# Optimization experiments

Hardware: AMD Instinct MI355X
Metric: run time of the kernel (lower is better)

## Reference

```python
import jax, jax.numpy as jnp
import numpy as np

N, E, R, H = 20000, 320000, 8, 4
KG, CC = 128, 4
IN, HID, OUT = 256, 256, 256  # in_channels = KG + 128 (GCN out)
HO1, HO2 = HID // H, OUT // H  # per-head out channels
SLOPE_ACT = 0.01   # nn.LeakyReLU default
SLOPE_ATT = 0.2    # RGATConv negative_slope default


def gcn_conv(x, W, b, src, dst):
    """PyG GCNConv: add self loops, symmetric norm, x@W, scatter-sum, +bias."""
    n = x.shape[0]
    loop = jnp.arange(n, dtype=src.dtype)
    s = jnp.concatenate([src, loop])
    d = jnp.concatenate([dst, loop])
    deg = jnp.zeros((n,), x.dtype).at[d].add(1.0)
    dis = jnp.where(deg > 0, jax.lax.rsqrt(jnp.maximum(deg, 1.0)), 0.0)
    norm = dis[s] * dis[d]                        # [E+N]
    h = x @ W                                     # [n, out]
    out = jax.ops.segment_sum(norm[:, None] * h[s], d, num_segments=n)
    return out + b


def rgat_conv(x, W, q, k, b, src, dst, edge_type, heads, oc):
    """PyG RGATConv (additive-self-attention, across-relation, dim=1, concat)."""
    n = x.shape[0]
    xw = jnp.einsum('ni,rio->rno', x, W)          # [R, n, heads*oc]
    out_i = xw[edge_type, dst]                    # [E, heads*oc]
    out_j = xw[edge_type, src]                    # [E, heads*oc]
    qi = out_i @ q                                # [E, heads]
    kj = out_j @ k                                # [E, heads]
    alpha = jax.nn.leaky_relu(qi + kj, SLOPE_ATT)
    # softmax over incoming edges per destination node (across-relation)
    amax = jax.ops.segment_max(alpha, dst, num_segments=n)[dst]
    ex = jnp.exp(alpha - amax)
    denom = jax.ops.segment_sum(ex, dst, num_segments=n)[dst]
    alpha = ex / denom                            # [E, heads]
    e = src.shape[0]
    msg = (alpha[:, :, None] * out_j.reshape(e, heads, oc)).reshape(e, heads * oc)
    out = jax.ops.segment_sum(msg, dst, num_segments=n) + b
    return out, alpha


def setup_inputs() -> dict:
    key = jax.random.key(0)
    ks = jax.random.split(key, 16)
    d = {}
    d['kg_emb'] = jax.random.normal(ks[0], (N, KG), jnp.float32)
    d['ccle0'] = jax.random.normal(ks[1], (N, CC), jnp.float32)
    d['gcn_w1'] = jax.random.normal(ks[2], (CC, 32), jnp.float32) / np.float32(np.sqrt(CC))
    d['gcn_b1'] = jnp.zeros((32,), jnp.float32)
    d['gcn_w2'] = jax.random.normal(ks[3], (32, 128), jnp.float32) / np.float32(np.sqrt(32))
    d['gcn_b2'] = jnp.zeros((128,), jnp.float32)
    d['rgat1_w'] = jax.random.normal(ks[4], (R, IN, HID), jnp.float32) / np.float32(np.sqrt(IN))
    d['rgat1_q'] = jax.random.normal(ks[5], (HID, H), jnp.float32) / np.float32(np.sqrt(HID))
    d['rgat1_k'] = jax.random.normal(ks[6], (HID, H), jnp.float32) / np.float32(np.sqrt(HID))
    d['rgat1_b'] = jnp.zeros((HID,), jnp.float32)
    d['rgat2_w'] = jax.random.normal(ks[7], (R, HID, OUT), jnp.float32) / np.float32(np.sqrt(HID))
    d['rgat2_q'] = jax.random.normal(ks[8], (OUT, H), jnp.float32) / np.float32(np.sqrt(OUT))
    d['rgat2_k'] = jax.random.normal(ks[9], (OUT, H), jnp.float32) / np.float32(np.sqrt(OUT))
    d['rgat2_b'] = jnp.zeros((OUT,), jnp.float32)
    d['lin_w'] = jax.random.normal(ks[10], (IN, OUT), jnp.float32) / np.float32(np.sqrt(IN))
    d['lin_b'] = jnp.zeros((OUT,), jnp.float32)
    d['edge_index'] = jax.random.randint(ks[11], (2, E), 0, N, jnp.int32)
    d['edge_type'] = jax.random.randint(ks[12], (E,), 0, R, jnp.int32)
    return d


def reference(kg_emb, ccle0, gcn_w1, gcn_b1, gcn_w2, gcn_b2,
              rgat1_w, rgat1_q, rgat1_k, rgat1_b,
              rgat2_w, rgat2_q, rgat2_k, rgat2_b,
              lin_w, lin_b, edge_index, edge_type):
    src, dst = edge_index[0], edge_index[1]
    # ccle_layer: GCN(4->32) -> LeakyReLU -> GCN(32->128)
    c = gcn_conv(ccle0, gcn_w1, gcn_b1, src, dst)
    c = jax.nn.leaky_relu(c, SLOPE_ACT)
    c = gcn_conv(c, gcn_w2, gcn_b2, src, dst)
    # node_id = arange(N): concat(kg_emb, ccle_out)
    x0 = jnp.concatenate([kg_emb, c], axis=1)     # [N, IN]
    h, a1 = rgat_conv(x0, rgat1_w, rgat1_q, rgat1_k, rgat1_b,
                      src, dst, edge_type, H, HO1)
    h = jax.nn.leaky_relu(h, SLOPE_ACT)           # dropout p=0 -> identity
    h, a2 = rgat_conv(h, rgat2_w, rgat2_q, rgat2_k, rgat2_b,
                      src, dst, edge_type, H, HO2)
    out = h + (x0 @ lin_w + lin_b)                # residual through self.lin
    return out, a1, a2
```

## Files before the change

### kernel.cpp

```cpp
#include <hip/hip_runtime.h>
#include <cstdint>

static constexpr int N = 20000;
static constexpr int E = 320000;
static constexpr int R = 8;
static constexpr int H = 4;
static constexpr int C = 256;

using short8 = __attribute__((ext_vector_type(8))) short;
using f32x4  = __attribute__((ext_vector_type(4))) float;

__device__ __forceinline__ float lrelu(float x, float s) { return x >= 0.f ? x : s * x; }
__device__ __forceinline__ unsigned short f2bf(float f) {
    unsigned u = __float_as_uint(f);
    unsigned r = (u + 0x7FFFu + ((u >> 16) & 1u)) >> 16;
    return (unsigned short)r;
}
__device__ __forceinline__ float bf2f(unsigned short s) {
    return __uint_as_float(((unsigned)s) << 16);
}

__global__ void k_zero_int(int* p, int n) {
    int i = blockIdx.x * blockDim.x + threadIdx.x;
    if (i < n) p[i] = 0;
}

__global__ void k_count(const int* __restrict__ ei, int* __restrict__ cnt) {
    int e = blockIdx.x * blockDim.x + threadIdx.x;
    if (e < E) atomicAdd(&cnt[ei[E + e]], 1);
}

__global__ __launch_bounds__(1024) void k_scan(const int* __restrict__ cnt,
                                               int* __restrict__ rowptr,
                                               int* __restrict__ cursor,
                                               float* __restrict__ dis) {
    __shared__ int part[1024];
    const int CH = (N + 1023) / 1024;
    int t = threadIdx.x;
    int base = t * CH;
    int sum = 0;
    for (int j = 0; j < CH; ++j) {
        int idx = base + j;
        if (idx < N) sum += cnt[idx];
    }
    part[t] = sum;
    __syncthreads();
    for (int off = 1; off < 1024; off <<= 1) {
        int v = 0;
        if (t >= off) v = part[t - off];
        __syncthreads();
        if (t >= off) part[t] += v;
        __syncthreads();
    }
    int run = part[t] - sum;
    for (int j = 0; j < CH; ++j) {
        int idx = base + j;
        if (idx < N) {
            int cv = cnt[idx];
            rowptr[idx] = run;
            cursor[idx] = run;
            dis[idx] = rsqrtf((float)cv + 1.0f);
            run += cv;
        }
    }
    if (t == 1023) rowptr[N] = part[1023];
}

__global__ void k_scatter(const int* __restrict__ ei, const int* __restrict__ et,
                          int* __restrict__ cursor, int* __restrict__ csr_se,
                          int* __restrict__ csr_eid) {
    int e = blockIdx.x * blockDim.x + threadIdx.x;
    if (e >= E) return;
    int d = ei[E + e];
    int pos = atomicAdd(&cursor[d], 1);
    csr_se[pos] = (et[e] << 16) | ei[e];
    csr_eid[pos] = e;
}

__global__ void k_h1(const float* __restrict__ x, const float* __restrict__ W,
                     float* __restrict__ h) {
    int idx = blockIdx.x * blockDim.x + threadIdx.x;
    if (idx >= N * 32) return;
    int n = idx >> 5, f = idx & 31;
    const float* xr = x + n * 4;
    float acc = 0.f;
#pragma unroll
    for (int c = 0; c < 4; ++c) acc += xr[c] * W[c * 32 + f];
    h[idx] = acc;
}

__global__ void k_agg32(const int* __restrict__ rowptr, const int* __restrict__ csr_se,
                        const float* __restrict__ dis, const float* __restrict__ h,
                        const float* __restrict__ b, float* __restrict__ c) {
    int idx = blockIdx.x * blockDim.x + threadIdx.x;
    if (idx >= N * 32) return;
    int d = idx >> 5, f = idx & 31;
    int beg = rowptr[d], end = rowptr[d + 1];
    float acc = 0.f;
    for (int i = beg; i < end; ++i) {
        int s = csr_se[i] & 0xFFFF;
        acc += dis[s] * h[s * 32 + f];
    }
    float dd = dis[d];
    c[idx] = dd * acc + dd * dd * h[idx] + b[f];
}

__global__ void k_h2kg(const float* __restrict__ c1, const float* __restrict__ W,
                       const float* __restrict__ kg, unsigned short* __restrict__ h,
                       float* __restrict__ x0, unsigned short* __restrict__ xb0) {
    int idx = blockIdx.x * blockDim.x + threadIdx.x;
    if (idx >= N * 128) return;
    int n = idx >> 7, f = idx & 127;
    const float* cr = c1 + n * 32;
    float acc = 0.f;
    for (int c = 0; c < 32; ++c) acc += lrelu(cr[c], 0.01f) * W[c * 128 + f];
    h[idx] = f2bf(acc);
    float v = kg[idx];
    x0[n * 256 + f] = v;
    xb0[n * 256 + f] = f2bf(v);
}

__global__ void k_agg128(const int* __restrict__ rowptr, const int* __restrict__ csr_se,
                         const float* __restrict__ dis,
                         const unsigned short* __restrict__ h,
                         const float* __restrict__ b, float* __restrict__ x0,
                         unsigned short* __restrict__ xb0) {
    int idx = blockIdx.x * blockDim.x + threadIdx.x;
    if (idx >= N * 128) return;
    int d = idx >> 7, f = idx & 127;
    int beg = rowptr[d], end = rowptr[d + 1];
    float acc = 0.f;
    int i = beg;
    for (; i + 2 <= end; i += 2) {
        int s0 = csr_se[i] & 0xFFFF;
        int s1 = csr_se[i + 1] & 0xFFFF;
        float d0 = dis[s0], d1 = dis[s1];
        float v0 = bf2f(h[s0 * 128 + f]), v1 = bf2f(h[s1 * 128 + f]);
        acc += d0 * v0 + d1 * v1;
    }
    if (i < end) {
        int s = csr_se[i] & 0xFFFF;
        acc += dis[s] * bf2f(h[s * 128 + f]);
    }
    float dd = dis[d];
    float v = dd * acc + dd * dd * bf2f(h[d * 128 + f]) + b[f];
    x0[d * 256 + 128 + f] = v;
    xb0[d * 256 + 128 + f] = f2bf(v);
}

__global__ __launch_bounds__(256) void k_wqkb(const float* __restrict__ W,
                                              const float* __restrict__ q,
                                              const float* __restrict__ kmat,
                                              unsigned short* __restrict__ wqkb) {
    int w = (blockIdx.x * blockDim.x + threadIdx.x) >> 6;
    int lane = threadIdx.x & 63;
    int r = w >> 8, i = w & 255;
    const float* wr = W + ((size_t)(r * 256 + i)) * 256;
    float4 a = *(const float4*)(wr + lane * 4);
    float aq0 = 0.f, aq1 = 0.f, aq2 = 0.f, aq3 = 0.f;
    float ak0 = 0.f, ak1 = 0.f, ak2 = 0.f, ak3 = 0.f;
    int o = lane * 4;
    const float av[4] = {a.x, a.y, a.z, a.w};
#pragma unroll
    for (int j = 0; j < 4; ++j) {
        float4 qv = *(const float4*)(q + (o + j) * 4);
        float4 kv = *(const float4*)(kmat + (o + j) * 4);
        aq0 += av[j] * qv.x; aq1 += av[j] * qv.y;
        aq2 += av[j] * qv.z; aq3 += av[j] * qv.w;
        ak0 += av[j] * kv.x; ak1 += av[j] * kv.y;
        ak2 += av[j] * kv.z; ak3 += av[j] * kv.w;
    }
#pragma unroll
    for (int d = 1; d < 64; d <<= 1) {
        aq0 += __shfl_xor(aq0, d); aq1 += __shfl_xor(aq1, d);
        aq2 += __shfl_xor(aq2, d); aq3 += __shfl_xor(aq3, d);
        ak0 += __shfl_xor(ak0, d); ak1 += __shfl_xor(ak1, d);
        ak2 += __shfl_xor(ak2, d); ak3 += __shfl_xor(ak3, d);
    }
    if (lane == 0) {
        int nq = r * 4, nk = 32 + r * 4;
        wqkb[(nq + 0) * 256 + i] = f2bf(aq0);
        wqkb[(nq + 1) * 256 + i] = f2bf(aq1);
        wqkb[(nq + 2) * 256 + i] = f2bf(aq2);
        wqkb[(nq + 3) * 256 + i] = f2bf(aq3);
        wqkb[(nk + 0) * 256 + i] = f2bf(ak0);
        wqkb[(nk + 1) * 256 + i] = f2bf(ak1);
        wqkb[(nk + 2) * 256 + i] = f2bf(ak2);
        wqkb[(nk + 3) * 256 + i] = f2bf(ak3);
    }
}

#define QP 264
__global__ __launch_bounds__(256) void k_qnkn_mfma(
    const unsigned short* __restrict__ xb, const unsigned short* __restrict__ wqkb,
    float* __restrict__ qn, float* __restrict__ kn)
{
    __shared__ unsigned short Ws[64 * QP];
    int t = threadIdx.x;
    {
        int r = t >> 2, off = (t & 3) * 64;
#pragma unroll
        for (int i = 0; i < 8; ++i)
            *(uint4*)(&Ws[r * QP + off + i * 8]) =
                *(const uint4*)(wqkb + r * 256 + off + i * 8);
    }
    __syncthreads();
    int wave = t >> 6, lane = t & 63;
    int lrow = lane & 15, kq = lane >> 4;
    int mw = blockIdx.x * 64 + wave * 16;
    int gm = mw + lrow;
    int gmc = gm < N ? gm : N - 1;

    f32x4 acc[4];
#pragma unroll
    for (int j = 0; j < 4; ++j) acc[j] = (f32x4){0.f, 0.f, 0.f, 0.f};

    for (int k0 = 0; k0 < 8; ++k0) {
        short8 af = *(const short8*)(xb + (size_t)gmc * 256 + k0 * 32 + kq * 8);
#pragma unroll
        for (int j = 0; j < 4; ++j) {
            short8 bf4 = *(const short8*)(&Ws[(j * 16 + lrow) * QP + k0 * 32 + kq * 8]);
            acc[j] = __builtin_amdgcn_mfma_f32_16x16x32_bf16(af, bf4, acc[j], 0, 0, 0);
        }
    }
#pragma unroll
    for (int j = 0; j < 4; ++j) {
        int col = j * 16 + lrow;
#pragma unroll
        for (int reg = 0; reg < 4; ++reg) {
            int gr = mw + kq * 4 + reg;
            if (gr < N) {
                if (col < 32) qn[gr * 32 + col] = acc[j][reg];
                else          kn[gr * 32 + (col - 32)] = acc[j][reg];
            }
        }
    }
}

__global__ void k_soft(const int* __restrict__ rowptr, const int* __restrict__ csr_se,
                       const int* __restrict__ csr_eid,
                       const float* __restrict__ qn, const float* __restrict__ kn,
                       float* __restrict__ alpha_csr, float* __restrict__ aout) {
    int wid = (blockIdx.x * blockDim.x + threadIdx.x) >> 6;
    int lane = threadIdx.x & 63;
    if (wid >= N) return;
    int d = wid;
    int beg = rowptr[d], end = rowptr[d + 1];
    if (beg >= end) return;
    int slot = lane >> 2, h = lane & 3;
    int nc = (end - beg + 15) >> 4;
    const float* qrow = qn + d * 32;

    auto rawv = [&](int i) {
        int se = csr_se[i];
        int tt = se >> 16, s = se & 0xFFFF;
        return lrelu(qrow[tt * 4 + h] + kn[s * 32 + tt * 4 + h], 0.2f);
    };

    float av[4];
    float m = -1e30f;
    for (int c = 0; c < nc; ++c) {
        int i = beg + c * 16 + slot;
        float v = (i < end) ? rawv(i) : -1e30f;
        if (c < 4) av[c] = v;
        m = fmaxf(m, v);
    }
    m = fmaxf(m, __shfl_xor(m, 4));
    m = fmaxf(m, __shfl_xor(m, 8));
    m = fmaxf(m, __shfl_xor(m, 16));
    m = fmaxf(m, __shfl_xor(m, 32));

    float sum = 0.f;
    for (int c = 0; c < nc; ++c) {
        int i = beg + c * 16 + slot;
        float ex = 0.f;
        if (i < end) {
            float v = (c < 4) ? av[c] : rawv(i);
            ex = expf(v - m);
        }
        if (c < 4) av[c] = ex;
        sum += ex;
    }
    sum += __shfl_xor(sum, 4);
    sum += __shfl_xor(sum, 8);
    sum += __shfl_xor(sum, 16);
    sum += __shfl_xor(sum, 32);
    float inv = 1.f / sum;

    for (int c = 0; c < nc; ++c) {
        int i = beg + c * 16 + slot;
        if (i < end) {
            float ex = (c < 4) ? av[c] : expf(rawv(i) - m);
            float a = ex * inv;
            alpha_csr[i * 4 + h] = a;
            aout[csr_eid[i] * 4 + h] = a;
        }
    }
}

#define WTP 72
__global__ __launch_bounds__(256) void k_wconv_t(const float* __restrict__ W,
                                                 unsigned short* __restrict__ Wt) {
    int bid = blockIdx.x;
    int z = bid >> 4;
    int tile = bid & 15;
    int k0 = (tile >> 2) * 64, n0 = (tile & 3) * 64;
    __shared__ unsigned short T[64 * WTP];
    int t = threadIdx.x;
    const float* Wz = W + ((size_t)z << 16);
    int r = t >> 4;
    int cs = (t & 15) * 4;
#pragma unroll
    for (int rr = 0; rr < 4; ++rr) {
        int k = r + rr * 16;
        float4 v = *(const float4*)(Wz + (size_t)(k0 + k) * 256 + n0 + cs);
        T[(cs + 0) * WTP + k] = f2bf(v.x);
        T[(cs + 1) * WTP + k] = f2bf(v.y);
        T[(cs + 2) * WTP + k] = f2bf(v.z);
        T[(cs + 3) * WTP + k] = f2bf(v.w);
    }
    __syncthreads();
    int n = t >> 2, ck = (t & 3) * 16;
    unsigned short* dst = Wt + ((size_t)z << 16) + (size_t)(n0 + n) * 256 + k0 + ck;
    const unsigned short* srcp = T + n * WTP + ck;
    *(uint4*)(dst) = *(const uint4*)(srcp);
    *(uint4*)(dst + 8) = *(const uint4*)(srcp + 8);
}

#define TM 128
#define TN 128
#define TK 32
#define LPP 40
__global__ __launch_bounds__(512) void gemm_mfma4(
    const unsigned short* __restrict__ A, const unsigned short* __restrict__ Bt,
    unsigned short* __restrict__ Cbf, float* __restrict__ Cf,
    const float* __restrict__ bias, const float* __restrict__ bias2,
    int M, int NZ, int NT, int MT, int zlin)
{
    __shared__ unsigned short As[TM * LPP];
    __shared__ unsigned short Bs[TN * LPP];

    int bi = blockIdx.x;
    int cx = bi & 7;
    int g = bi >> 3;
    int per = NZ * NT;
    int mh = g / per;
    int j  = g % per;
    int mt = mh * 8 + cx;
    if (mt >= MT) return;
    int z  = j % NZ;
    int nb = j / NZ;
    int m0 = mt * TM;
    int n0 = nb * TN;

    const unsigned short* Bz = Bt + ((size_t)z << 16);
    int t = threadIdx.x;
    int wave = t >> 6, lane = t & 63;
    int wr = wave >> 2;
    int wc = wave & 3;
    int lrow = lane & 15, kq = lane >> 4;
    int srow = t >> 2, skc = t & 3;

    f32x4 acc[4][2];
#pragma unroll
    for (int i = 0; i < 4; ++i)
#pragma unroll
        for (int jj = 0; jj < 2; ++jj) acc[i][jj] = (f32x4){0.f, 0.f, 0.f, 0.f};

    for (int k0 = 0; k0 < 256; k0 += TK) {
        {
            int gm = m0 + srow;
            uint4 va = {0, 0, 0, 0};
            if (gm < M) va = *(const uint4*)(A + (size_t)gm * 256 + k0 + skc * 8);
            *(uint4*)(&As[srow * LPP + skc * 8]) = va;
            uint4 vb = *(const uint4*)(Bz + (size_t)(n0 + srow) * 256 + k0 + skc * 8);
            *(uint4*)(&Bs[srow * LPP + skc * 8]) = vb;
        }
        __syncthreads();
        short8 af[4], bf4[2];
#pragma unroll
        for (int i = 0; i < 4; ++i)
            af[i] = *(const short8*)(&As[(wr * 64 + i * 16 + lrow) * LPP + kq * 8]);
#pragma unroll
        for (int jj = 0; jj < 2; ++jj)
            bf4[jj] = *(const short8*)(&Bs[(wc * 32 + jj * 16 + lrow) * LPP + kq * 8]);
#pragma unroll
        for (int i = 0; i < 4; ++i)
#pragma unroll
            for (int jj = 0; jj < 2; ++jj)
                acc[i][jj] = __builtin_amdgcn_mfma_f32_16x16x32_bf16(af[i], bf4[jj],
                                                                     acc[i][jj], 0, 0, 0);
        __syncthreads();
    }
    if (z == zlin) {
#pragma unroll
        for (int i = 0; i < 4; ++i)
#pragma unroll
            for (int jj = 0; jj < 2; ++jj) {
                int gn = n0 + wc * 32 + jj * 16 + lrow;
                float bsum = bias[gn] + bias2[gn];
#pragma unroll
                for (int reg = 0; reg < 4; ++reg) {
                    int gm = m0 + wr * 64 + i * 16 + kq * 4 + reg;
                    if (gm < M) Cf[(size_t)gm * 256 + gn] = acc[i][jj][reg] + bsum;
                }
            }
    } else {
#pragma unroll
        for (int i = 0; i < 4; ++i)
#pragma unroll
            for (int jj = 0; jj < 2; ++jj) {
                int gn = n0 + wc * 32 + jj * 16 + lrow;
#pragma unroll
                for (int reg = 0; reg < 4; ++reg) {
                    int gm = m0 + wr * 64 + i * 16 + kq * 4 + reg;
                    if (gm < M)
                        Cbf[((size_t)z * M + gm) * 256 + gn] = f2bf(acc[i][jj][reg]);
                }
            }
    }
}

__global__ __launch_bounds__(256) void k_msg_gather(
    const int* __restrict__ rowptr, const int* __restrict__ csr_se,
    const float* __restrict__ alpha_csr, const unsigned short* __restrict__ xw,
    const float* __restrict__ bias, float* __restrict__ out,
    unsigned short* __restrict__ xbout, int r0, int r1, int first, int act) {
    __shared__ float Pf[2][256];
    int tid = threadIdx.x;
    int wave = tid >> 6, lane = tid & 63;
    int nslot = wave >> 1, p = wave & 1;
    int node = blockIdx.x * 2 + nslot;
    int hsel = lane >> 4;
    float ax = 0.f, ay = 0.f, az = 0.f, aw = 0.f;

    auto edge = [&](int i) {
        int se = csr_se[i];
        int tt = se >> 16;
        if (tt >= r0 && tt < r1) {
            int s = se & 0xFFFF;
            float a = alpha_csr[i * 4 + hsel];
            uint2 pv = *(const uint2*)(xw + ((size_t)(tt - r0) * N + s) * 256 + lane * 4);
            ax += a * __uint_as_float(pv.x << 16);
            ay += a * __uint_as_float(pv.x & 0xFFFF0000u);
            az += a * __uint_as_float(pv.y << 16);
            aw += a * __uint_as_float(pv.y & 0xFFFF0000u);
        }
    };

    if (node < N) {
        int beg = rowptr[node], end = rowptr[node + 1];
        int i = beg + p;
        for (; i + 2 < end; i += 4) { edge(i); edge(i + 2); }
        if (i < end) edge(i);
    }
    if (p == 1) {
        float4 v = {ax, ay, az, aw};
        *(float4*)(&Pf[nslot][lane * 4]) = v;
    }
    __syncthreads();
    if (p == 0 && node < N) {
        float4 q = *(const float4*)(&Pf[nslot][lane * 4]);
        ax += q.x; ay += q.y; az += q.z; aw += q.w;
        float* o = out + (size_t)node * 256 + lane * 4;
        float vx, vy, vz, vw;
        if (first) {
            const float4 b = ((const float4*)bias)[lane];
            vx = ax + b.x; vy = ay + b.y; vz = az + b.z; vw = aw + b.w;
        } else {
            vx = o[0] + ax; vy = o[1] + ay; vz = o[2] + az; vw = o[3] + aw;
        }
        if (act) {
            vx = lrelu(vx, 0.01f); vy = lrelu(vy, 0.01f);
            vz = lrelu(vz, 0.01f); vw = lrelu(vw, 0.01f);
            unsigned short* xo = xbout + (size_t)node * 256 + lane * 4;
            xo[0] = f2bf(vx); xo[1] = f2bf(vy); xo[2] = f2bf(vz); xo[3] = f2bf(vw);
        }
        o[0] = vx; o[1] = vy; o[2] = vz; o[3] = vw;
    }
}

extern "C" void kernel_launch(void* const* d_in, const int* in_sizes, int n_in,
                              void* d_out, int out_size, void* d_ws, size_t ws_size,
                              hipStream_t stream) {
    const float* kg   = (const float*)d_in[0];
    const float* cc0  = (const float*)d_in[1];
    const float* gw1  = (const float*)d_in[2];
    const float* gb1  = (const float*)d_in[3];
    const float* gw2  = (const float*)d_in[4];
    const float* gb2  = (const float*)d_in[5];
    const float* r1w  = (const float*)d_in[6];
    const float* r1q  = (const float*)d_in[7];
    const float* r1k  = (const float*)d_in[8];
    const float* r1b  = (const float*)d_in[9];
    const float* r2w  = (const float*)d_in[10];
    const float* r2q  = (const float*)d_in[11];
    const float* r2k  = (const float*)d_in[12];
    const float* r2b  = (const float*)d_in[13];
    const float* linw = (const float*)d_in[14];
    const float* linb = (const float*)d_in[15];
    const int*   ei   = (const int*)d_in[16];
    const int*   et   = (const int*)d_in[17];

    float* out = (float*)d_out;
    float* a1  = out + (size_t)N * C;
    float* a2  = a1 + (size_t)E * H;

    float* ws = (float*)d_ws;
    size_t off = 0;
    float* dis  = ws + off; off += N;
    float* h1   = ws + off; off += (size_t)N * 32;
    float* c1   = ws + off; off += (size_t)N * 32;
    unsigned short* h2b = (unsigned short*)(ws + off); off += (size_t)N * 64;
    float* x0   = ws + off; off += (size_t)N * C;
    float* hmid = ws + off; off += (size_t)N * C;
    float* qn   = ws + off; off += (size_t)N * R * H;
    float* kn   = ws + off; off += (size_t)N * R * H;
    int* cnt     = (int*)(ws + off); off += N;
    int* rowptr  = (int*)(ws + off); off += N + 1;
    int* cursor  = (int*)(ws + off); off += N;
    int* csr_se  = (int*)(ws + off); off += E;
    int* csr_eid = (int*)(ws + off); off += E;
    float* alpha = ws + off; off += (size_t)E * H;
    unsigned short* xb0 = (unsigned short*)(ws + off); off += (size_t)N * 128;
    unsigned short* xb1 = (unsigned short*)(ws + off); off += (size_t)N * 128;
    unsigned short* wt  = (unsigned short*)(ws + off); off += (size_t)(R + 1) * 32768;
    unsigned short* wtl = wt + ((size_t)R << 16);
    unsigned short* wqkb = (unsigned short*)(ws + off); off += 8192;
    unsigned short* xwb = (unsigned short*)(ws + off);

    size_t fixedB = off * 4;
    int K = R;
    if (ws_size > fixedB) {
        size_t kmax = (ws_size - fixedB) / ((size_t)N * C * 2);
        if (kmax < (size_t)K) K = (int)kmax;
    } else {
        K = 1;
    }
    if (K < 1) K = 1;

    const int B = 256;
    auto cdiv = [](long a, long b) { return (int)((a + b - 1) / b); };
    const int MT = cdiv(N, TM);
    const int NT = C / TN;

    k_zero_int<<<cdiv(N, B), B, 0, stream>>>(cnt, N);
    k_count<<<cdiv(E, B), B, 0, stream>>>(ei, cnt);
    k_scan<<<1, 1024, 0, stream>>>(cnt, rowptr, cursor, dis);
    k_scatter<<<cdiv(E, B), B, 0, stream>>>(ei, et, cursor, csr_se, csr_eid);

    k_h1<<<cdiv((long)N * 32, B), B, 0, stream>>>(cc0, gw1, h1);
    k_agg32<<<cdiv((long)N * 32, B), B, 0, stream>>>(rowptr, csr_se, dis, h1, gb1, c1);
    k_h2kg<<<cdiv((long)N * 128, B), B, 0, stream>>>(c1, gw2, kg, h2b, x0, xb0);
    k_agg128<<<cdiv((long)N * 128, B), B, 0, stream>>>(rowptr, csr_se, dis, h2b,
                                                       gb2, x0, xb0);

    auto rgat = [&](unsigned short* xb, const float* W,
                    const float* q, const float* kk, const float* b,
                    float* obuf, unsigned short* xbout, float* aout,
                    int first, int act, int lin, float* linout,
                    const float* lb1, const float* lb2) {
        k_wqkb<<<512, 256, 0, stream>>>(W, q, kk, wqkb);
        k_qnkn_mfma<<<cdiv(N, 64), B, 0, stream>>>(xb, wqkb, qn, kn);
        k_soft<<<cdiv((long)N * 64, B), B, 0, stream>>>(rowptr, csr_se, csr_eid,
                                                        qn, kn, alpha, aout);
        k_wconv_t<<<R * 16, 256, 0, stream>>>(W, wt);
        for (int r0 = 0; r0 < R; r0 += K) {
            int kc = (R - r0) < K ? (R - r0) : K;
            int addlin = (lin && (r0 + kc == R)) ? 1 : 0;
            int nz = kc + addlin;
            int zl = addlin ? kc : -1;
            int gx = 8 * nz * NT * cdiv(MT, 8);
            gemm_mfma4<<<gx, 512, 0, stream>>>(xb, wt + ((size_t)r0 << 16), xwb,
                                               linout, lb1, lb2,
                                               N, nz, NT, MT, zl);
            int last = (r0 + kc >= R) ? 1 : 0;
            k_msg_gather<<<cdiv(N, 2), 256, 0, stream>>>(
                rowptr, csr_se, alpha, xwb, b, obuf, xbout, r0, r0 + kc,
                (first && r0 == 0) ? 1 : 0, act && last);
        }
    };

    k_wconv_t<<<16, 256, 0, stream>>>(linw, wtl);

    rgat(xb0, r1w, r1q, r1k, r1b, hmid, xb1, a1, 1, 1,
         1, out, linb, r2b);

    rgat(xb1, r2w, r2q, r2k, r2b, out, nullptr, a2, 0, 0,
         0, nullptr, nullptr, nullptr);
}
```

Baseline: 528.8 us.

## Use direct global-to-LDS loads and 256-thread 4x4-fragment GEMM tiles

The bf16 MFMA GEMM now stages A and B tiles with global_load_lds (buffer-to-LDS DMA, 16 bytes per lane), so data no longer passes through registers. The LDS pad is dropped and the block shrinks from 512 to 256 threads, each wave computing a 64x64 sub-tile (4x4 MFMA fragments) instead of 64x32. Out-of-range rows are clamped to the last valid row rather than zero-filled. The unpadded LDS layout may cause bank conflicts on fragment reads, and each wave now holds more accumulators, which raises register pressure.

```diff
diff --git a/kernel.cpp b/kernel.cpp
--- a/kernel.cpp
+++ b/kernel.cpp
@@ -18,6 +18,12 @@
 }
 __device__ __forceinline__ float bf2f(unsigned short s) {
     return __uint_as_float(((unsigned)s) << 16);
+}
+
+__device__ __forceinline__ void gl2l16(const unsigned short* g, unsigned short* l) {
+    __builtin_amdgcn_global_load_lds(
+        (const __attribute__((address_space(1))) unsigned int*)g,
+        (__attribute__((address_space(3))) unsigned int*)l, 16, 0, 0);
 }
 
 __global__ void k_zero_int(int* p, int n) {
@@ -329,16 +335,14 @@
 
 #define TM 128
 #define TN 128
-#define TK 32
-#define LPP 40
-__global__ __launch_bounds__(512) void gemm_mfma4(
+__global__ __launch_bounds__(256) void gemm_mfma4(
     const unsigned short* __restrict__ A, const unsigned short* __restrict__ Bt,
     unsigned short* __restrict__ Cbf, float* __restrict__ Cf,
     const float* __restrict__ bias, const float* __restrict__ bias2,
     int M, int NZ, int NT, int MT, int zlin)
 {
-    __shared__ unsigned short As[TM * LPP];
-    __shared__ unsigned short Bs[TN * LPP];
+    __shared__ unsigned short As[128 * 32];
+    __shared__ unsigned short Bs[128 * 32];
 
     int bi = blockIdx.x;
     int cx = bi & 7;
@@ -356,38 +360,46 @@
     const unsigned short* Bz = Bt + ((size_t)z << 16);
     int t = threadIdx.x;
     int wave = t >> 6, lane = t & 63;
-    int wr = wave >> 2;
-    int wc = wave & 3;
+    int wr = wave >> 1, wc = wave & 1;
     int lrow = lane & 15, kq = lane >> 4;
-    int srow = t >> 2, skc = t & 3;
-
-    f32x4 acc[4][2];
+
+    int sr0 = (wave * 2 + 0) * 16 + (lane >> 2);
+    int sr1 = (wave * 2 + 1) * 16 + (lane >> 2);
+    int sc = (lane & 3) * 8;
+    int gm0 = m0 + sr0; if (gm0 >= M) gm0 = M - 1;
+    int gm1 = m0 + sr1; if (gm1 >= M) gm1 = M - 1;
+    const unsigned short* gA0 = A + (size_t)gm0 * 256 + sc;
+    const unsigned short* gA1 = A + (size_t)gm1 * 256 + sc;
+    const unsigned short* gB0 = Bz + (size_t)(n0 + sr0) * 256 + sc;
+    const unsigned short* gB1 = Bz + (size_t)(n0 + sr1) * 256 + sc;
+    unsigned short* lA0 = &As[(wave * 2 + 0) * 512];
+    unsigned short* lA1 = &As[(wave * 2 + 1) * 512];
+    unsigned short* lB0 = &Bs[(wave * 2 + 0) * 512];
+    unsigned short* lB1 = &Bs[(wave * 2 + 1) * 512];
+
+    f32x4 acc[4][4];
 #pragma unroll
     for (int i = 0; i < 4; ++i)
 #pragma unroll
-        for (int jj = 0; jj < 2; ++jj) acc[i][jj] = (f32x4){0.f, 0.f, 0.f, 0.f};
-
-    for (int k0 = 0; k0 < 256; k0 += TK) {
-        {
-            int gm = m0 + srow;
-            uint4 va = {0, 0, 0, 0};
-            if (gm < M) va = *(const uint4*)(A + (size_t)gm * 256 + k0 + skc * 8);
-            *(uint4*)(&As[srow * LPP + skc * 8]) = va;
-            uint4 vb = *(const uint4*)(Bz + (size_t)(n0 + srow) * 256 + k0 + skc * 8);
-            *(uint4*)(&Bs[srow * LPP + skc * 8]) = vb;
-        }
+        for (int jj = 0; jj < 4; ++jj) acc[i][jj] = (f32x4){0.f, 0.f, 0.f, 0.f};
+
+    for (int k0 = 0; k0 < 256; k0 += 32) {
+        gl2l16(gA0 + k0, lA0);
+        gl2l16(gA1 + k0, lA1);
+        gl2l16(gB0 + k0, lB0);
+        gl2l16(gB1 + k0, lB1);
         __syncthreads();
-        short8 af[4], bf4[2];
+        short8 af[4], bf4[4];
 #pragma unroll
         for (int i = 0; i < 4; ++i)
-            af[i] = *(const short8*)(&As[(wr * 64 + i * 16 + lrow) * LPP + kq * 8]);
-#pragma unroll
-        for (int jj = 0; jj < 2; ++jj)
-            bf4[jj] = *(const short8*)(&Bs[(wc * 32 + jj * 16 + lrow) * LPP + kq * 8]);
+            af[i] = *(const short8*)(&As[(wr * 64 + i * 16 + lrow) * 32 + kq * 8]);
+#pragma unroll
+        for (int jj = 0; jj < 4; ++jj)
+            bf4[jj] = *(const short8*)(&Bs[(wc * 64 + jj * 16 + lrow) * 32 + kq * 8]);
 #pragma unroll
         for (int i = 0; i < 4; ++i)
 #pragma unroll
-            for (int jj = 0; jj < 2; ++jj)
+            for (int jj = 0; jj < 4; ++jj)
                 acc[i][jj] = __builtin_amdgcn_mfma_f32_16x16x32_bf16(af[i], bf4[jj],
                                                                      acc[i][jj], 0, 0, 0);
         __syncthreads();
@@ -396,8 +408,8 @@
 #pragma unroll
         for (int i = 0; i < 4; ++i)
 #pragma unroll
-            for (int jj = 0; jj < 2; ++jj) {
-                int gn = n0 + wc * 32 + jj * 16 + lrow;
+            for (int jj = 0; jj < 4; ++jj) {
+                int gn = n0 + wc * 64 + jj * 16 + lrow;
                 float bsum = bias[gn] + bias2[gn];
 #pragma unroll
                 for (int reg = 0; reg < 4; ++reg) {
@@ -409,8 +421,8 @@
 #pragma unroll
         for (int i = 0; i < 4; ++i)
 #pragma unroll
-            for (int jj = 0; jj < 2; ++jj) {
-                int gn = n0 + wc * 32 + jj * 16 + lrow;
+            for (int jj = 0; jj < 4; ++jj) {
+                int gn = n0 + wc * 64 + jj * 16 + lrow;
 #pragma unroll
                 for (int reg = 0; reg < 4; ++reg) {
                     int gm = m0 + wr * 64 + i * 16 + kq * 4 + reg;
@@ -571,7 +583,7 @@
             int nz = kc + addlin;
             int zl = addlin ? kc : -1;
             int gx = 8 * nz * NT * cdiv(MT, 8);
-            gemm_mfma4<<<gx, 512, 0, stream>>>(xb, wt + ((size_t)r0 << 16), xwb,
+            gemm_mfma4<<<gx, 256, 0, stream>>>(xb, wt + ((size_t)r0 << 16), xwb,
                                                linout, lb1, lb2,
                                                N, nz, NT, MT, zl);
             int last = (r0 + kc >= R) ? 1 : 0;
```

New measurement: 518.2 us. 1.02x faster.
